# Optimization experiments

Hardware: AMD Instinct MI355X
Metric: run time of the kernel (lower is better)

Reference implementation:

```python
import jax, jax.numpy as jnp
import numpy as np

EPS = 1e-5
NUM_HEADS = 8


def setup_inputs() -> dict:
    key = jax.random.key(0)
    ks = jax.random.split(key, 6)
    B, C, S = 4, 512, 2048
    std = 0.02
    return {
        "hidden_states": jax.random.normal(ks[0], (B, C, S), dtype=jnp.float32),
        "gn_weight": jnp.ones((C,), dtype=jnp.float32),
        "gn_bias": jnp.zeros((C,), dtype=jnp.float32),
        "wq": jax.random.normal(ks[1], (C, C), dtype=jnp.float32) * std,
        "bq": jnp.zeros((C,), dtype=jnp.float32),
        "wk": jax.random.normal(ks[2], (C, C), dtype=jnp.float32) * std,
        "bk": jnp.zeros((C,), dtype=jnp.float32),
        "wv": jax.random.normal(ks[3], (C, C), dtype=jnp.float32) * std,
        "bv": jnp.zeros((C,), dtype=jnp.float32),
        "wo": jax.random.normal(ks[4], (C, C), dtype=jnp.float32) * std,
        "bo": jnp.zeros((C,), dtype=jnp.float32),
    }


def reference(hidden_states, gn_weight, gn_bias, wq, bq, wk, bk, wv, bv, wo, bo):
    # hidden_states: [B, C, S]
    x = hidden_states
    B, C, S = x.shape
    H = NUM_HEADS
    D = C // H

    # GroupNorm with 1 group: normalize over (C, S) per sample
    mean = jnp.mean(x, axis=(1, 2), keepdims=True)
    var = jnp.var(x, axis=(1, 2), keepdims=True)
    h = (x - mean) * jax.lax.rsqrt(var + EPS)
    h = h * gn_weight[None, :, None] + gn_bias[None, :, None]

    h = jnp.swapaxes(h, 1, 2)  # [B, S, C]

    q = h @ wq.T + bq  # [B, S, C]
    k = h @ wk.T + bk
    v = h @ wv.T + bv

    # split heads: [B, H, S, D]
    q = q.reshape(B, S, H, D).transpose(0, 2, 1, 3)
    k = k.reshape(B, S, H, D).transpose(0, 2, 1, 3)
    v = v.reshape(B, S, H, D).transpose(0, 2, 1, 3)

    scale = 1.0 / (D ** 0.25)  # applied to both q and k, as in source
    scores = jnp.einsum('bhqd,bhkd->bhqk', q * scale, k * scale)
    probs = jax.nn.softmax(scores, axis=-1)
    out = jnp.einsum('bhqk,bhkd->bhqd', probs, v)  # [B, H, S, D]

    out = out.transpose(0, 2, 1, 3).reshape(B, S, C)  # [B, S, C]
    out = out @ wo.T + bo
    out = jnp.swapaxes(out, 1, 2)  # [B, C, S]
    return out + hidden_states
```

## Files before the change

### kernel.cpp

```cpp
#include <hip/hip_runtime.h>

typedef __attribute__((ext_vector_type(8))) __bf16 bf16x8;
typedef __attribute__((ext_vector_type(4))) __bf16 bf16x4;
typedef __attribute__((ext_vector_type(4))) float f32x4;
typedef __attribute__((ext_vector_type(16))) float f32x16;

#define BSZ 4
#define CCH 512
#define SEQ 2048
#define NH  8
#define HD  64

__device__ __forceinline__ f32x4 mfma16(bf16x8 a, bf16x8 b, f32x4 c) {
  return __builtin_amdgcn_mfma_f32_16x16x32_bf16(a, b, c, 0, 0, 0);
}
__device__ __forceinline__ f32x16 mfma32(bf16x8 a, bf16x8 b, f32x16 c) {
  return __builtin_amdgcn_mfma_f32_32x32x16_bf16(a, b, c, 0, 0, 0);
}

__device__ __forceinline__ void gload16(const void* g, void* l) {
  __builtin_amdgcn_global_load_lds((const __attribute__((address_space(1))) void*)g,
                                   (__attribute__((address_space(3))) void*)l,
                                   16, 0, 0);
}

__device__ __forceinline__ unsigned cvtpk(float lo, float hi) {
  unsigned r;
  asm("v_cvt_pk_bf16_f32 %0, %1, %2" : "=v"(r) : "v"(lo), "v"(hi));
  return r;
}
__device__ __forceinline__ void pl32swap(unsigned& a, unsigned& b) {
  asm("v_permlane32_swap_b32 %0, %1" : "+v"(a), "+v"(b));
}

#define WAIT_VM(N)                                          \
  asm volatile("s_waitcnt vmcnt(" #N ")" ::: "memory");     \
  __builtin_amdgcn_sched_barrier(0);                        \
  __builtin_amdgcn_s_barrier();

__global__ __launch_bounds__(256) void gn_partial(const float* __restrict__ x,
                                                  float* __restrict__ stats) {
  int b = blockIdx.y;
  const float4* xb = (const float4*)(x + ((size_t)b << 20) + (size_t)blockIdx.x * 16384);
  int tid = threadIdx.x;
  float s = 0.f, sq = 0.f;
#pragma unroll
  for (int i = 0; i < 16; ++i) {
    float4 v = xb[i * 256 + tid];
    s  += v.x + v.y + v.z + v.w;
    sq += v.x * v.x + v.y * v.y + v.z * v.z + v.w * v.w;
  }
#pragma unroll
  for (int o = 32; o > 0; o >>= 1) { s += __shfl_down(s, o); sq += __shfl_down(sq, o); }
  __shared__ float ls[4], lq[4];
  int w = tid >> 6;
  if ((tid & 63) == 0) { ls[w] = s; lq[w] = sq; }
  __syncthreads();
  if (tid == 0) {
    stats[b * 64 + blockIdx.x]       = ls[0] + ls[1] + ls[2] + ls[3];
    stats[256 + b * 64 + blockIdx.x] = lq[0] + lq[1] + lq[2] + lq[3];
  }
}

__global__ __launch_bounds__(256) void norm_tr(const float* __restrict__ x,
                                               const float* __restrict__ gw,
                                               const float* __restrict__ gb,
                                               const float* __restrict__ stats,
                                               __bf16* __restrict__ h) {
  int s0 = blockIdx.x * 64, c0 = blockIdx.y * 64, b = blockIdx.z;
  float sacc = 0.f, qacc = 0.f;
  for (int i = 0; i < 64; ++i) {
    sacc += stats[b * 64 + i];
    qacc += stats[256 + b * 64 + i];
  }
  const float inv_n = 1.0f / 1048576.f;
  float mean = sacc * inv_n;
  float rstd = rsqrtf(qacc * inv_n - mean * mean + 1e-5f);
  const float* xb = x + ((size_t)b << 20);
  __shared__ __align__(16) __bf16 tile[64][72];
  int tid = threadIdx.x;
#pragma unroll
  for (int j = 0; j < 16; ++j) {
    int e = tid + j * 256;
    int cl = e >> 6, sl = e & 63;
    float vv = xb[(size_t)(c0 + cl) * 2048 + s0 + sl];
    float hn = (vv - mean) * rstd * gw[c0 + cl] + gb[c0 + cl];
    tile[cl][sl] = (__bf16)hn;
  }
  __syncthreads();
#pragma unroll
  for (int j = 0; j < 2; ++j) {
    int row = (tid >> 3) + j * 32;
    int cg = tid & 7;
    bf16x8 pk;
#pragma unroll
    for (int e = 0; e < 8; ++e) pk[e] = tile[cg * 8 + e][row];
    *(bf16x8*)&h[(size_t)((b << 11) + s0 + row) * 512 + c0 + cg * 8] = pk;
  }
}

__global__ __launch_bounds__(256) void wcvt(const float* __restrict__ wq, const float* __restrict__ wk,
                                            const float* __restrict__ wv, const float* __restrict__ wo,
                                            __bf16* __restrict__ out) {
  int i = blockIdx.x * 256 + threadIdx.x;
  out[i]          = (__bf16)wq[i];
  out[262144 + i] = (__bf16)wk[i];
  out[524288 + i] = (__bf16)wv[i];
  out[786432 + i] = (__bf16)wo[i];
}

__global__ __launch_bounds__(256) void gemm_qkv(const __bf16* __restrict__ A, const __bf16* __restrict__ Wb,
                                                const float* __restrict__ bq, const float* __restrict__ bk,
                                                const float* __restrict__ bvv,
                                                __bf16* __restrict__ oq, __bf16* __restrict__ ok,
                                                __bf16* __restrict__ ovt) {
  __shared__ __align__(16) union QU {
    struct SS { __bf16 a[2][8192]; __bf16 b[2][8192]; } s;
    __bf16 t[128 * 136];
  } u;
  int z = blockIdx.z;
  const __bf16* W = Wb + (size_t)z * 262144;
  const float* bias = z == 0 ? bq : (z == 1 ? bk : bvv);
  int tid = threadIdx.x, wid = tid >> 6, l = tid & 63;
  int m0 = blockIdx.x * 128, n0 = blockIdx.y * 128;
  int wm = (wid >> 1) * 64, wn = (wid & 1) * 64;
  int l16 = l & 15, lg = l >> 4;
  f32x4 zero = {0.f, 0.f, 0.f, 0.f};
  f32x4 acc[4][4];
#pragma unroll
  for (int mt = 0; mt < 4; ++mt)
#pragma unroll
    for (int nt = 0; nt < 4; ++nt) acc[mt][nt] = zero;

  int rloc = l >> 3;
  int sg = ((l & 7) ^ rloc) * 8;
  int rdx = l16 & 7;

  auto STG = [&](int buf, int k0) {
#pragma unroll
    for (int t = 0; t < 4; ++t) {
      int row = wid * 32 + t * 8;
      gload16(A + (size_t)(m0 + row + rloc) * 512 + k0 + sg, &u.s.a[buf][row * 64]);
      gload16(W + (size_t)(n0 + row + rloc) * 512 + k0 + sg, &u.s.b[buf][row * 64]);
    }
  };
  auto CMP = [&](int buf) {
#pragma unroll
    for (int kk = 0; kk < 2; ++kk) {
      bf16x8 af[4], bfr[4];
#pragma unroll
      for (int mt = 0; mt < 4; ++mt)
        af[mt] = *(const bf16x8*)&u.s.a[buf][(wm + mt * 16 + l16) * 64 + (((kk * 4 + lg) ^ rdx) * 8)];
#pragma unroll
      for (int nt = 0; nt < 4; ++nt)
        bfr[nt] = *(const bf16x8*)&u.s.b[buf][(wn + nt * 16 + l16) * 64 + (((kk * 4 + lg) ^ rdx) * 8)];
      __builtin_amdgcn_s_setprio(1);
#pragma unroll
      for (int mt = 0; mt < 4; ++mt)
#pragma unroll
        for (int nt = 0; nt < 4; ++nt) acc[mt][nt] = mfma16(af[mt], bfr[nt], acc[mt][nt]);
      __builtin_amdgcn_s_setprio(0);
    }
  };

  STG(0, 0);
  WAIT_VM(0);
#pragma unroll
  for (int t = 0; t < 8; ++t) {
    if (t < 7) STG((t + 1) & 1, (t + 1) * 64);
    CMP(t & 1);
    if (t < 7) { WAIT_VM(0); }
  }

  if (z < 2) {
    __bf16* out = z == 0 ? oq : ok;
#pragma unroll
    for (int nt = 0; nt < 4; ++nt) {
      int col = n0 + wn + nt * 16 + l16;
      float bb = bias[col];
#pragma unroll
      for (int mt = 0; mt < 4; ++mt)
#pragma unroll
        for (int r = 0; r < 4; ++r)
          out[(size_t)(m0 + wm + mt * 16 + lg * 4 + r) * 512 + col] = (__bf16)(acc[mt][nt][r] + bb);
    }
  } else {
    __syncthreads();
#pragma unroll
    for (int nt = 0; nt < 4; ++nt) {
      int col = wn + nt * 16 + l16;
      float bb = bias[n0 + col];
#pragma unroll
      for (int mt = 0; mt < 4; ++mt)
#pragma unroll
        for (int r = 0; r < 4; ++r)
          u.t[col * 136 + wm + mt * 16 + lg * 4 + r] = (__bf16)(acc[mt][nt][r] + bb);
    }
    __syncthreads();
    int bI = m0 >> 11, sbase = m0 & 2047;
#pragma unroll
    for (int p = 0; p < 8; ++p) {
      int row = (tid >> 4) + p * 16;
      int ck = tid & 15;
      bf16x8 v = *(const bf16x8*)&u.t[row * 136 + ck * 8];
      int colg = n0 + row;
      int hd = colg >> 6, dd = colg & 63;
      *(bf16x8*)&ovt[((size_t)((bI * 8 + hd) * 64 + dd)) * 2048 + sbase + ck * 8] = v;
    }
  }
}

__global__ __launch_bounds__(256) void attn(const __bf16* __restrict__ q, const __bf16* __restrict__ k,
                                            const __bf16* __restrict__ vt, __bf16* __restrict__ ao) {
  const float C2 = 0.18033688011f;
  int tid = threadIdx.x, w = tid >> 6, l = tid & 63;
  int q0w = blockIdx.x * 128 + w * 32;
  int hh = blockIdx.y, b = blockIdx.z;
  int l31 = l & 31, hi = l >> 5;

  __shared__ __align__(16) __bf16 smem[3][8192];

  bf16x8 qf[4];
  {
    const __bf16* qrow = q + ((size_t)((b << 11) + q0w + l31)) * 512 + hh * 64 + hi * 8;
#pragma unroll
    for (int dt = 0; dt < 4; ++dt) qf[dt] = *(const bf16x8*)&qrow[dt * 16];
  }
  bf16x8 ones;
#pragma unroll
  for (int j = 0; j < 8; ++j) ones[j] = (__bf16)1.0f;

  const __bf16* kbase = k + ((size_t)(b << 11)) * 512 + hh * 64;
  const __bf16* vtb = vt + ((size_t)((b * 8 + hh) * 64)) * 2048;

  f32x16 zero16 = {};
  f32x16 o2[2];
  o2[0] = zero16; o2[1] = zero16;
  f32x16 facc = zero16;

  int rloc = l >> 3;
  int swz = (l31 & 7);
  int q3 = (l31 >> 3) & 3;

  auto STAGE = [&](int buf, int kv0) {
#pragma unroll
    for (int i = 0; i < 4; ++i) {
      int c = w * 4 + i;
      int cc = c & 7;
      int row = cc * 8 + rloc;
      int sg = (((l & 7) ^ rloc ^ (cc & 3))) * 8;
      if (c < 8) {
        gload16(kbase + (size_t)(kv0 + row) * 512 + sg, &smem[buf][c * 512]);
      } else {
        gload16(vtb + (size_t)row * 2048 + kv0 + sg, &smem[buf][4096 + cc * 512]);
      }
    }
  };

  auto COMPUTE = [&](int buf) {
    const __bf16* Kt = &smem[buf][0];
    const __bf16* Vts = &smem[buf][4096];
    f32x16 sc[2];
#pragma unroll
    for (int kb = 0; kb < 2; ++kb) {
      sc[kb] = zero16;
      int r = kb * 32 + l31;
      __builtin_amdgcn_s_setprio(1);
#pragma unroll
      for (int dt = 0; dt < 4; ++dt) {
        bf16x8 kf = *(const bf16x8*)&Kt[r * 64 + ((dt * 2 + hi) ^ swz ^ q3) * 8];
        sc[kb] = mfma32(kf, qf[dt], sc[kb]);
      }
      __builtin_amdgcn_s_setprio(0);
    }

#pragma unroll
    for (int kb = 0; kb < 2; ++kb)
#pragma unroll
      for (int r = 0; r < 16; ++r)
        sc[kb][r] = exp2f(sc[kb][r] * C2);

#pragma unroll
    for (int t = 0; t < 4; ++t) {
      int kb = t >> 1, h8 = (t & 1) * 8;
      unsigned u0 = cvtpk(sc[kb][h8 + 0], sc[kb][h8 + 1]);
      unsigned u1 = cvtpk(sc[kb][h8 + 2], sc[kb][h8 + 3]);
      unsigned u2 = cvtpk(sc[kb][h8 + 4], sc[kb][h8 + 5]);
      unsigned u3 = cvtpk(sc[kb][h8 + 6], sc[kb][h8 + 7]);
      pl32swap(u0, u2);
      pl32swap(u1, u3);
      union { unsigned u[4]; bf16x8 v; } pb;
      pb.u[0] = u0; pb.u[1] = u1; pb.u[2] = u2; pb.u[3] = u3;
      __builtin_amdgcn_s_setprio(1);
      facc = mfma32(ones, pb.v, facc);
#pragma unroll
      for (int dblk = 0; dblk < 2; ++dblk) {
        int r = dblk * 32 + l31;
        bf16x8 vf = *(const bf16x8*)&Vts[r * 64 + ((t * 2 + hi) ^ swz ^ q3) * 8];
        o2[dblk] = mfma32(vf, pb.v, o2[dblk]);
      }
      __builtin_amdgcn_s_setprio(0);
    }
  };

  STAGE(0, 0);
  STAGE(1, 64);
  int bc = 0, sb = 2;
  for (int t = 0; t < 31; ++t) {
    WAIT_VM(4);
    if (t < 30) { STAGE(sb, (t + 2) * 64); sb = sb == 2 ? 0 : sb + 1; }
    COMPUTE(bc); bc = bc == 2 ? 0 : bc + 1;
  }
  WAIT_VM(0);
  COMPUTE(bc);

  float invl = 1.0f / facc[0];
  __bf16* T = &smem[0][w * 2048];
  int swzq = (l31 & 7) * 8;
#pragma unroll
  for (int dblk = 0; dblk < 2; ++dblk)
#pragma unroll
    for (int g = 0; g < 4; ++g) {
      unsigned w0 = cvtpk(o2[dblk][g * 4 + 0] * invl, o2[dblk][g * 4 + 1] * invl);
      unsigned w1 = cvtpk(o2[dblk][g * 4 + 2] * invl, o2[dblk][g * 4 + 3] * invl);
      int d4 = dblk * 32 + g * 8 + hi * 4;
      uint2 pk2; pk2.x = w0; pk2.y = w1;
      *(uint2*)&T[l31 * 64 + (d4 ^ swzq)] = pk2;
    }
  int qr = l >> 1, hf = l & 1;
  int swzr = (qr & 7) * 8;
  __bf16* aorow = ao + (size_t)((b << 11) + q0w + qr) * 512 + hh * 64;
#pragma unroll
  for (int m = 0; m < 2; ++m) {
    int e = hf * 32 + m * 16;
    bf16x8 v0 = *(const bf16x8*)&T[qr * 64 + ((e) ^ swzr)];
    bf16x8 v1 = *(const bf16x8*)&T[qr * 64 + ((e + 8) ^ swzr)];
    *(bf16x8*)&aorow[e] = v0;
    *(bf16x8*)&aorow[e + 8] = v1;
  }
}

__global__ __launch_bounds__(256) void gemm_proj(const __bf16* __restrict__ A, const __bf16* __restrict__ W,
                                                 const float* __restrict__ bias,
                                                 const float* __restrict__ resid,
                                                 float* __restrict__ outp) {
  __shared__ __align__(16) union UU {
    struct SS { __bf16 a[2][8192]; __bf16 b[2][8192]; } s;
    float st[128 * 129];
  } u;
  int tid = threadIdx.x, wid = tid >> 6, l = tid & 63;
  int m0 = blockIdx.x * 128, n0 = blockIdx.y * 128;
  int wm = (wid >> 1) * 64, wn = (wid & 1) * 64;
  int l16 = l & 15, lg = l >> 4;
  f32x4 zero = {0.f, 0.f, 0.f, 0.f};
  f32x4 acc[4][4];
#pragma unroll
  for (int mt = 0; mt < 4; ++mt)
#pragma unroll
    for (int nt = 0; nt < 4; ++nt) acc[mt][nt] = zero;

  int rloc = l >> 3;
  int sg = ((l & 7) ^ rloc) * 8;
  int rdx = l16 & 7;

  auto STG = [&](int buf, int k0) {
#pragma unroll
    for (int t = 0; t < 4; ++t) {
      int row = wid * 32 + t * 8;
      gload16(A + (size_t)(m0 + row + rloc) * 512 + k0 + sg, &u.s.a[buf][row * 64]);
      gload16(W + (size_t)(n0 + row + rloc) * 512 + k0 + sg, &u.s.b[buf][row * 64]);
    }
  };
  auto CMP = [&](int buf) {
#pragma unroll
    for (int kk = 0; kk < 2; ++kk) {
      bf16x8 af[4], bfr[4];
#pragma unroll
      for (int mt = 0; mt < 4; ++mt)
        af[mt] = *(const bf16x8*)&u.s.a[buf][(wm + mt * 16 + l16) * 64 + (((kk * 4 + lg) ^ rdx) * 8)];
#pragma unroll
      for (int nt = 0; nt < 4; ++nt)
        bfr[nt] = *(const bf16x8*)&u.s.b[buf][(wn + nt * 16 + l16) * 64 + (((kk * 4 + lg) ^ rdx) * 8)];
      __builtin_amdgcn_s_setprio(1);
#pragma unroll
      for (int mt = 0; mt < 4; ++mt)
#pragma unroll
        for (int nt = 0; nt < 4; ++nt) acc[mt][nt] = mfma16(af[mt], bfr[nt], acc[mt][nt]);
      __builtin_amdgcn_s_setprio(0);
    }
  };

  STG(0, 0);
  WAIT_VM(0);
#pragma unroll
  for (int t = 0; t < 8; ++t) {
    if (t < 7) STG((t + 1) & 1, (t + 1) * 64);
    CMP(t & 1);
    if (t < 7) { WAIT_VM(0); }
  }

  __syncthreads();
#pragma unroll
  for (int nt = 0; nt < 4; ++nt) {
    int col = wn + nt * 16 + l16;
    float bb = bias[n0 + col];
#pragma unroll
    for (int mt = 0; mt < 4; ++mt)
#pragma unroll
      for (int r = 0; r < 4; ++r)
        u.st[(wm + mt * 16 + lg * 4 + r) * 129 + col] = acc[mt][nt][r] + bb;
  }
  __syncthreads();
  int b = m0 >> 11;
  int sbase = m0 & 2047;
  const float* rb = resid + ((size_t)b << 20);
  float* ob = outp + ((size_t)b << 20);
#pragma unroll
  for (int it = 0; it < 16; ++it) {
    int c = (tid >> 5) + it * 8;
    int s4 = (tid & 31) * 4;
    float4 r4 = *(const float4*)&rb[(size_t)(n0 + c) * 2048 + sbase + s4];
    float4 o4;
    o4.x = u.st[(s4 + 0) * 129 + c] + r4.x;
    o4.y = u.st[(s4 + 1) * 129 + c] + r4.y;
    o4.z = u.st[(s4 + 2) * 129 + c] + r4.z;
    o4.w = u.st[(s4 + 3) * 129 + c] + r4.w;
    *(float4*)&ob[(size_t)(n0 + c) * 2048 + sbase + s4] = o4;
  }
}

extern "C" void kernel_launch(void* const* d_in, const int* in_sizes, int n_in,
                              void* d_out, int out_size, void* d_ws, size_t ws_size,
                              hipStream_t stream) {
  const float* x   = (const float*)d_in[0];
  const float* gw  = (const float*)d_in[1];
  const float* gb  = (const float*)d_in[2];
  const float* wqf = (const float*)d_in[3];
  const float* bqf = (const float*)d_in[4];
  const float* wkf = (const float*)d_in[5];
  const float* bkf = (const float*)d_in[6];
  const float* wvf = (const float*)d_in[7];
  const float* bvf = (const float*)d_in[8];
  const float* wof = (const float*)d_in[9];
  const float* bof = (const float*)d_in[10];
  float* outp = (float*)d_out;

  char* ws = (char*)d_ws;
  float* stats = (float*)ws;
  const size_t MAT = (size_t)8192 * 512;
  __bf16* h  = (__bf16*)(ws + 4096);
  __bf16* q  = h + MAT;
  __bf16* k  = q + MAT;
  __bf16* vt = k + MAT;
  __bf16* ao = vt + MAT;
  __bf16* wB = ao + MAT;

  gn_partial<<<dim3(64, 4), 256, 0, stream>>>(x, stats);
  norm_tr<<<dim3(32, 8, 4), 256, 0, stream>>>(x, gw, gb, stats, h);
  wcvt<<<1024, 256, 0, stream>>>(wqf, wkf, wvf, wof, wB);
  gemm_qkv<<<dim3(64, 4, 3), 256, 0, stream>>>(h, wB, bqf, bkf, bvf, q, k, vt);
  attn<<<dim3(16, 8, 4), 256, 0, stream>>>(q, k, vt, ao);
  gemm_proj<<<dim3(64, 4), 256, 0, stream>>>(ao, wB + 3 * 262144, bof, x, outp);
}
```

Baseline: 191.1 us.

## Split attention over KV halves with a combine pass; shrink QKV GEMM K-tile

Attention now splits the key/value sequence into two halves across blockIdx.z, doubling the grid to 1024 blocks. Each half writes unnormalized fp32 partial outputs and row sums, and a new combine kernel adds them and normalizes to bf16. The attention pipeline drops from triple to double buffering with __syncthreads, which lowers LDS use. The QKV GEMM K-tile is halved to 32 with a new swizzle and twice as many steps. The split adds fp32 partial-output traffic and an extra launch in exchange for more parallelism. It appears to rely on both halves sharing one softmax max offset, or on no max subtraction at all.

```diff
diff --git a/kernel.cpp b/kernel.cpp
--- a/kernel.cpp
+++ b/kernel.cpp
@@ -115,7 +115,7 @@
                                                 __bf16* __restrict__ oq, __bf16* __restrict__ ok,
                                                 __bf16* __restrict__ ovt) {
   __shared__ __align__(16) union QU {
-    struct SS { __bf16 a[2][8192]; __bf16 b[2][8192]; } s;
+    struct SS { __bf16 a[2][4096]; __bf16 b[2][4096]; } s;
     __bf16 t[128 * 136];
   } u;
   int z = blockIdx.z;
@@ -132,44 +132,38 @@
 #pragma unroll
     for (int nt = 0; nt < 4; ++nt) acc[mt][nt] = zero;
 
-  int rloc = l >> 3;
-  int sg = ((l & 7) ^ rloc) * 8;
-  int rdx = l16 & 7;
+  int srow = wid * 32 + (l >> 2);
+  int scol = ((l & 3) ^ ((l >> 3) & 3)) * 8;
+  int rs = (lg ^ ((l16 >> 1) & 3)) * 8;
 
   auto STG = [&](int buf, int k0) {
 #pragma unroll
-    for (int t = 0; t < 4; ++t) {
-      int row = wid * 32 + t * 8;
-      gload16(A + (size_t)(m0 + row + rloc) * 512 + k0 + sg, &u.s.a[buf][row * 64]);
-      gload16(W + (size_t)(n0 + row + rloc) * 512 + k0 + sg, &u.s.b[buf][row * 64]);
+    for (int t = 0; t < 2; ++t) {
+      gload16(A + (size_t)(m0 + srow + t * 16) * 512 + k0 + scol, &u.s.a[buf][(wid * 32 + t * 16) * 32]);
+      gload16(W + (size_t)(n0 + srow + t * 16) * 512 + k0 + scol, &u.s.b[buf][(wid * 32 + t * 16) * 32]);
     }
   };
   auto CMP = [&](int buf) {
-#pragma unroll
-    for (int kk = 0; kk < 2; ++kk) {
-      bf16x8 af[4], bfr[4];
-#pragma unroll
-      for (int mt = 0; mt < 4; ++mt)
-        af[mt] = *(const bf16x8*)&u.s.a[buf][(wm + mt * 16 + l16) * 64 + (((kk * 4 + lg) ^ rdx) * 8)];
-#pragma unroll
-      for (int nt = 0; nt < 4; ++nt)
-        bfr[nt] = *(const bf16x8*)&u.s.b[buf][(wn + nt * 16 + l16) * 64 + (((kk * 4 + lg) ^ rdx) * 8)];
-      __builtin_amdgcn_s_setprio(1);
-#pragma unroll
-      for (int mt = 0; mt < 4; ++mt)
-#pragma unroll
-        for (int nt = 0; nt < 4; ++nt) acc[mt][nt] = mfma16(af[mt], bfr[nt], acc[mt][nt]);
-      __builtin_amdgcn_s_setprio(0);
-    }
+    bf16x8 af[4], bfr[4];
+#pragma unroll
+    for (int mt = 0; mt < 4; ++mt) af[mt] = *(const bf16x8*)&u.s.a[buf][(wm + mt * 16 + l16) * 32 + rs];
+#pragma unroll
+    for (int nt = 0; nt < 4; ++nt) bfr[nt] = *(const bf16x8*)&u.s.b[buf][(wn + nt * 16 + l16) * 32 + rs];
+    __builtin_amdgcn_s_setprio(1);
+#pragma unroll
+    for (int mt = 0; mt < 4; ++mt)
+#pragma unroll
+      for (int nt = 0; nt < 4; ++nt) acc[mt][nt] = mfma16(af[mt], bfr[nt], acc[mt][nt]);
+    __builtin_amdgcn_s_setprio(0);
   };
 
   STG(0, 0);
   WAIT_VM(0);
 #pragma unroll
-  for (int t = 0; t < 8; ++t) {
-    if (t < 7) STG((t + 1) & 1, (t + 1) * 64);
+  for (int t = 0; t < 16; ++t) {
+    if (t < 15) STG((t + 1) & 1, (t + 1) * 32);
     CMP(t & 1);
-    if (t < 7) { WAIT_VM(0); }
+    if (t < 15) { WAIT_VM(0); }
   }
 
   if (z < 2) {
@@ -211,14 +205,17 @@
 }
 
 __global__ __launch_bounds__(256) void attn(const __bf16* __restrict__ q, const __bf16* __restrict__ k,
-                                            const __bf16* __restrict__ vt, __bf16* __restrict__ ao) {
+                                            const __bf16* __restrict__ vt,
+                                            float* __restrict__ opart, float* __restrict__ lpart) {
   const float C2 = 0.18033688011f;
   int tid = threadIdx.x, w = tid >> 6, l = tid & 63;
   int q0w = blockIdx.x * 128 + w * 32;
-  int hh = blockIdx.y, b = blockIdx.z;
+  int hh = blockIdx.y;
+  int z = blockIdx.z, b = z & 3, half = z >> 2;
+  int kvbase = half * 1024;
   int l31 = l & 31, hi = l >> 5;
 
-  __shared__ __align__(16) __bf16 smem[3][8192];
+  __shared__ __align__(16) __bf16 smem[2][8192];
 
   bf16x8 qf[4];
   {
@@ -303,41 +300,66 @@
     }
   };
 
-  STAGE(0, 0);
-  STAGE(1, 64);
-  int bc = 0, sb = 2;
-  for (int t = 0; t < 31; ++t) {
-    WAIT_VM(4);
-    if (t < 30) { STAGE(sb, (t + 2) * 64); sb = sb == 2 ? 0 : sb + 1; }
-    COMPUTE(bc); bc = bc == 2 ? 0 : bc + 1;
-  }
-  WAIT_VM(0);
-  COMPUTE(bc);
-
-  float invl = 1.0f / facc[0];
-  __bf16* T = &smem[0][w * 2048];
+  STAGE(0, kvbase);
+  __syncthreads();
+  int cur = 0;
+#pragma unroll 1
+  for (int t = 0; t < 16; ++t) {
+    if (t + 1 < 16) STAGE(cur ^ 1, kvbase + (t + 1) * 64);
+    COMPUTE(cur);
+    __syncthreads();
+    cur ^= 1;
+  }
+
+  float* T = (float*)&smem[0][0] + w * 2048;
   int swzq = (l31 & 7) * 8;
 #pragma unroll
   for (int dblk = 0; dblk < 2; ++dblk)
 #pragma unroll
     for (int g = 0; g < 4; ++g) {
-      unsigned w0 = cvtpk(o2[dblk][g * 4 + 0] * invl, o2[dblk][g * 4 + 1] * invl);
-      unsigned w1 = cvtpk(o2[dblk][g * 4 + 2] * invl, o2[dblk][g * 4 + 3] * invl);
+      float4 v4;
+      v4.x = o2[dblk][g * 4 + 0]; v4.y = o2[dblk][g * 4 + 1];
+      v4.z = o2[dblk][g * 4 + 2]; v4.w = o2[dblk][g * 4 + 3];
       int d4 = dblk * 32 + g * 8 + hi * 4;
-      uint2 pk2; pk2.x = w0; pk2.y = w1;
-      *(uint2*)&T[l31 * 64 + (d4 ^ swzq)] = pk2;
+      *(float4*)&T[l31 * 64 + (d4 ^ swzq)] = v4;
     }
   int qr = l >> 1, hf = l & 1;
   int swzr = (qr & 7) * 8;
-  __bf16* aorow = ao + (size_t)((b << 11) + q0w + qr) * 512 + hh * 64;
-#pragma unroll
-  for (int m = 0; m < 2; ++m) {
-    int e = hf * 32 + m * 16;
-    bf16x8 v0 = *(const bf16x8*)&T[qr * 64 + ((e) ^ swzr)];
-    bf16x8 v1 = *(const bf16x8*)&T[qr * 64 + ((e + 8) ^ swzr)];
-    *(bf16x8*)&aorow[e] = v0;
-    *(bf16x8*)&aorow[e + 8] = v1;
-  }
+  float* orow = opart + ((size_t)half << 22) + (size_t)((b << 11) + q0w + qr) * 512 + hh * 64;
+#pragma unroll
+  for (int m = 0; m < 8; ++m) {
+    int c = hf * 32 + m * 4;
+    float4 v = *(const float4*)&T[qr * 64 + (c ^ swzr)];
+    *(float4*)&orow[c] = v;
+  }
+  if (hi == 0)
+    lpart[((size_t)(half * 4 + b) * 8 + hh) * 2048 + q0w + l31] = facc[0];
+}
+
+__global__ __launch_bounds__(256) void combine(const float* __restrict__ opart,
+                                               const float* __restrict__ lpart,
+                                               __bf16* __restrict__ ao) {
+  size_t e = ((size_t)blockIdx.x * 256 + threadIdx.x) * 8;
+  int row = (int)(e >> 9);
+  int c = (int)(e & 511);
+  int b = row >> 11, s = row & 2047, hh = c >> 6;
+  float l0 = lpart[((size_t)b * 8 + hh) * 2048 + s];
+  float l1 = lpart[((size_t)(4 + b) * 8 + hh) * 2048 + s];
+  float inv = 1.0f / (l0 + l1);
+  float4 a0 = *(const float4*)&opart[e];
+  float4 a1 = *(const float4*)&opart[(1ull << 22) + e];
+  float4 c0 = *(const float4*)&opart[e + 4];
+  float4 c1 = *(const float4*)&opart[(1ull << 22) + e + 4];
+  bf16x8 o;
+  o[0] = (__bf16)((a0.x + a1.x) * inv);
+  o[1] = (__bf16)((a0.y + a1.y) * inv);
+  o[2] = (__bf16)((a0.z + a1.z) * inv);
+  o[3] = (__bf16)((a0.w + a1.w) * inv);
+  o[4] = (__bf16)((c0.x + c1.x) * inv);
+  o[5] = (__bf16)((c0.y + c1.y) * inv);
+  o[6] = (__bf16)((c0.z + c1.z) * inv);
+  o[7] = (__bf16)((c0.w + c1.w) * inv);
+  *(bf16x8*)&ao[e] = o;
 }
 
 __global__ __launch_bounds__(256) void gemm_proj(const __bf16* __restrict__ A, const __bf16* __restrict__ W,
@@ -454,11 +476,14 @@
   __bf16* vt = k + MAT;
   __bf16* ao = vt + MAT;
   __bf16* wB = ao + MAT;
+  float* opart = (float*)(wB + 4 * 262144);
+  float* lpart = opart + 2 * MAT;
 
   gn_partial<<<dim3(64, 4), 256, 0, stream>>>(x, stats);
   norm_tr<<<dim3(32, 8, 4), 256, 0, stream>>>(x, gw, gb, stats, h);
   wcvt<<<1024, 256, 0, stream>>>(wqf, wkf, wvf, wof, wB);
   gemm_qkv<<<dim3(64, 4, 3), 256, 0, stream>>>(h, wB, bqf, bkf, bvf, q, k, vt);
-  attn<<<dim3(16, 8, 4), 256, 0, stream>>>(q, k, vt, ao);
+  attn<<<dim3(16, 8, 8), 256, 0, stream>>>(q, k, vt, opart, lpart);
+  combine<<<2048, 256, 0, stream>>>(opart, lpart, ao);
   gemm_proj<<<dim3(64, 4), 256, 0, stream>>>(ao, wB + 3 * 262144, bof, x, outp);
 }
```

New measurement: 206.7 us. 8.2% more time.
